# Kernel tuning notes

Hardware: AMD Instinct MI355X
Metric: run time of the kernel (lower is better)

Reference implementation:

```python
import jax, jax.numpy as jnp
import numpy as np

B, S, V, P = 16, 100, 50000, 45
WE, PE, H = 100, 50, 400
H2 = 2 * H  # bilstm output size


def _lstm(x, Wih, Whh, b):
    """Unidirectional LSTM over time. x: [B,S,D] -> h: [B,S,H]. PyTorch gate order i,f,g,o."""
    Hs = Whh.shape[1]
    def step(carry, xt):
        h, c = carry
        g = xt @ Wih.T + h @ Whh.T + b
        i, f, gg, o = jnp.split(g, 4, axis=-1)
        c = jax.nn.sigmoid(f) * c + jax.nn.sigmoid(i) * jnp.tanh(gg)
        h = jax.nn.sigmoid(o) * jnp.tanh(c)
        return (h, c), h
    Bn = x.shape[0]
    init = (jnp.zeros((Bn, Hs), x.dtype), jnp.zeros((Bn, Hs), x.dtype))
    _, hs = jax.lax.scan(step, init, jnp.swapaxes(x, 0, 1))
    return jnp.swapaxes(hs, 0, 1)


def _bilstm_layer(x, Wf_ih, Wf_hh, bf, Wb_ih, Wb_hh, bb):
    hf = _lstm(x, Wf_ih, Wf_hh, bf)
    hb = _lstm(x[:, ::-1, :], Wb_ih, Wb_hh, bb)[:, ::-1, :]
    return jnp.concatenate([hf, hb], axis=-1)


def setup_inputs() -> dict:
    key = jax.random.key(0)
    ks = jax.random.split(key, 24)
    def n(k, shape, s=0.1):
        return jax.random.normal(k, shape, jnp.float32) * s
    inp = {
        "input_tokens": jax.random.randint(ks[0], (B, S), 0, V),
        "input_pos": jax.random.randint(ks[1], (B, S), 0, P),
        "input_head": jax.random.randint(ks[2], (B, S), 0, S),
        "word_W": n(ks[3], (V, WE)),
        "pos_W": n(ks[4], (P, PE)),
        "l0f_Wih": n(ks[5], (4 * H, WE + PE)), "l0f_Whh": n(ks[6], (4 * H, H)), "l0f_b": n(ks[7], (4 * H,)),
        "l0b_Wih": n(ks[8], (4 * H, WE + PE)), "l0b_Whh": n(ks[9], (4 * H, H)), "l0b_b": n(ks[10], (4 * H,)),
        "l1f_Wih": n(ks[11], (4 * H, H2)), "l1f_Whh": n(ks[12], (4 * H, H)), "l1f_b": n(ks[13], (4 * H,)),
        "l1b_Wih": n(ks[14], (4 * H, H2)), "l1b_Whh": n(ks[15], (4 * H, H)), "l1b_b": n(ks[16], (4 * H,)),
        "ua_W": n(ks[17], (H2, H2)), "ua_b": n(ks[18], (H2,)),
        "wa_W": n(ks[19], (H2, H2)), "wa_b": n(ks[20], (H2,)),
        "va_W": n(ks[21], (H2,)),
    }
    return inp


def reference(input_tokens, input_pos, input_head, word_W, pos_W,
              l0f_Wih, l0f_Whh, l0f_b, l0b_Wih, l0b_Whh, l0b_b,
              l1f_Wih, l1f_Whh, l1f_b, l1b_Wih, l1b_Whh, l1b_b,
              ua_W, ua_b, wa_W, wa_b, va_W):
    # embeddings (dropout is identity at eval)
    x = jnp.concatenate([word_W[input_tokens], pos_W[input_pos]], axis=-1)  # [B,S,150]
    h1 = _bilstm_layer(x, l0f_Wih, l0f_Whh, l0f_b, l0b_Wih, l0b_Whh, l0b_b)   # [B,S,H2]
    out = _bilstm_layer(h1, l1f_Wih, l1f_Whh, l1f_b, l1b_Wih, l1b_Whh, l1b_b)  # [B,S,H2]

    # batched additive biaffine scoring for targets i = 1..S-1 over all source positions j
    ua = out @ ua_W.T + ua_b  # u_a(source)  [B,S,H2]
    wa = out @ wa_W.T + wa_b  # w_a(target)  [B,S,H2]
    # g[b,t,j] = v_a . tanh(ua[b,j] + wa[b,t+1])
    g = jnp.einsum('btjh,h->btj', jnp.tanh(ua[:, None, :, :] + wa[:, 1:, None, :]), va_W)  # [B,S-1,S]
    # mask: output[:, j, 0] == output[:, i, 0]  (masks self, matching torch's output.eq(target)[:,:,0])
    mask = out[:, 1:, 0][:, :, None] == out[:, :, 0][:, None, :]  # [B,S-1,S]
    g = jnp.where(mask, -10000.0, g)
    logp = jax.nn.log_softmax(g, axis=2)  # log_softmax over source positions (torch dim=1)

    # loss: sum over i of NLLLoss(mean over batch, ignore_index=-1)
    gold = input_head[:, 1:]  # [B,S-1]
    valid = (gold != -1)
    nll = -jnp.take_along_axis(logp, jnp.clip(gold, 0, S - 1)[:, :, None], axis=2)[..., 0]
    nll = nll * valid.astype(logp.dtype)
    denom = jnp.maximum(valid.sum(axis=0), 1).astype(logp.dtype)
    loss = jnp.sum(nll.sum(axis=0) / denom)

    parent_prob_table = jnp.exp(logp)  # [B,S-1,S]
    preds = jnp.argmax(parent_prob_table, axis=2)  # [B,S-1]
    return (loss, preds, parent_prob_table)
```

## Files before the change

kernel.cpp:

```cpp
#include <hip/hip_runtime.h>

#define BB 16
#define SS 100
#define HH 400
#define H2 800
#define G4 1600
#define DIN0 150
#define KP0 160

#define OFF_GF   240000ULL
#define OFF_GB   2800000ULL
#define OFF_H1   5360000ULL
#define OFF_OUT2 6640000ULL
#define OFF_NLL  8078400ULL
#define OFF_EXH  8081600ULL
#define EX_U16_PER_PLANE 1331200ULL

typedef _Float16 f16x8 __attribute__((ext_vector_type(8)));
typedef float    f32x4 __attribute__((ext_vector_type(4)));
typedef unsigned long long u64x2 __attribute__((ext_vector_type(2)));

static __device__ __forceinline__ unsigned chkp(unsigned long long q) {
    return ((unsigned)q == 0xFFFFFFFFu) | ((unsigned)(q >> 32) == 0xFFFFFFFFu);
}
static __device__ __forceinline__ unsigned long long sanq(unsigned long long q) {
    if ((unsigned)q == 0xFFFFFFFFu)         q &= 0xFFFFFFFF00000000ull;
    if ((unsigned)(q >> 32) == 0xFFFFFFFFu) q &= 0x00000000FFFFFFFFull;
    return q;
}

static __device__ __forceinline__ void cvt8(const float* v, f16x8& hi, f16x8& lo)
{
#pragma unroll
    for (int i = 0; i < 8; i++) {
        _Float16 h = (_Float16)v[i];
        hi[i] = h;
        lo[i] = (_Float16)((v[i] - (float)h) * 2048.f);
    }
}
static __device__ __forceinline__ void cvt_pair8(float4 a, float4 b,
                                                 f16x8& hi, f16x8& lo)
{
    float v[8] = {a.x, a.y, a.z, a.w, b.x, b.y, b.z, b.w};
    cvt8(v, hi, lo);
}

#define AROW 40

__global__ __launch_bounds__(256) void gemm_l0_embed_dual(
    const int* __restrict__ tok, const int* __restrict__ pos,
    const float* __restrict__ wW, const float* __restrict__ pW,
    const float* __restrict__ W0, const float* __restrict__ b0, float* __restrict__ C0,
    const float* __restrict__ W1, const float* __restrict__ b1, float* __restrict__ C1,
    unsigned int* __restrict__ poison, int poison_words)
{
    {
        int nthreads = gridDim.x * gridDim.y * 256;
        int gtid = (blockIdx.y * gridDim.x + blockIdx.x) * 256 + threadIdx.x;
        for (int i = gtid; i < poison_words; i += nthreads) poison[i] = 0xFFFFFFFFu;
    }

    int half = gridDim.x >> 1;
    int sel = blockIdx.x >= half;
    int bx = blockIdx.x - (sel ? half : 0);
    const float* W = sel ? W1 : W0;
    const float* bias = sel ? b1 : b0;
    float* C = sel ? C1 : C0;

    int tid = threadIdx.x;
    int wv = tid >> 6, l = tid & 63;
    int lm = l & 15, lk = l >> 4;
    int rs = bx * 64 + wv * 16;
    int n0 = blockIdx.y * 64;

    __shared__ __attribute__((aligned(16))) unsigned short AhiS[2][64 * AROW];
    __shared__ __attribute__((aligned(16))) unsigned short AloS[2][64 * AROW];

    int sr = tid >> 2, sc = (tid & 3) * 8;
    int t_ = tok[n0 + sr], p_ = pos[n0 + sr];

    const float* wrow = W + (size_t)(rs + lm) * DIN0;

    f32x4 accH[4], accX[4];
#pragma unroll
    for (int ct = 0; ct < 4; ct++) {
        accH[ct] = {0.f, 0.f, 0.f, 0.f};
        accX[ct] = {0.f, 0.f, 0.f, 0.f};
    }

    float a8[8];
#pragma unroll
    for (int e = 0; e < 8; e++) {
        int k = sc + e;
        a8[e] = (k < 100) ? wW[t_ * 100 + k]
              : (k < DIN0) ? pW[p_ * 50 + (k - 100)] : 0.f;
    }
    float w8[8];
#pragma unroll
    for (int e = 0; e < 8; e++) {
        int k = lk * 8 + e;
        w8[e] = (k < DIN0) ? wrow[k] : 0.f;
    }
    {
        f16x8 h, lo2; cvt8(a8, h, lo2);
        *(f16x8*)&AhiS[0][sr * AROW + sc] = h;
        *(f16x8*)&AloS[0][sr * AROW + sc] = lo2;
    }

    const int nkt = 5;
    for (int kt = 0; kt < nkt; kt++) {
        __syncthreads();
        bool more = (kt + 1 < nkt);
        float a8n[8], w8n[8];
        if (more) {
            int kb = (kt + 1) << 5;
#pragma unroll
            for (int e = 0; e < 8; e++) {
                int k = kb + sc + e;
                a8n[e] = (k < 100) ? wW[t_ * 100 + k]
                       : (k < DIN0) ? pW[p_ * 50 + (k - 100)] : 0.f;
            }
#pragma unroll
            for (int e = 0; e < 8; e++) {
                int k = kb + lk * 8 + e;
                w8n[e] = (k < DIN0) ? wrow[k] : 0.f;
            }
        }
        f16x8 wh, wl; cvt8(w8, wh, wl);
        int buf = kt & 1;
#pragma unroll
        for (int ct = 0; ct < 4; ct++) {
            f16x8 ah = *(const f16x8*)&AhiS[buf][(ct * 16 + lm) * AROW + lk * 8];
            f16x8 al = *(const f16x8*)&AloS[buf][(ct * 16 + lm) * AROW + lk * 8];
            accH[ct] = __builtin_amdgcn_mfma_f32_16x16x32_f16(wh, ah, accH[ct], 0, 0, 0);
            accX[ct] = __builtin_amdgcn_mfma_f32_16x16x32_f16(wh, al, accX[ct], 0, 0, 0);
            accX[ct] = __builtin_amdgcn_mfma_f32_16x16x32_f16(wl, ah, accX[ct], 0, 0, 0);
        }
        if (more) {
            f16x8 h, lo2; cvt8(a8n, h, lo2);
            *(f16x8*)&AhiS[buf ^ 1][sr * AROW + sc] = h;
            *(f16x8*)&AloS[buf ^ 1][sr * AROW + sc] = lo2;
#pragma unroll
            for (int e = 0; e < 8; e++) w8[e] = w8n[e];
        }
    }

    float4 bv = *(const float4*)&bias[rs + lk * 4];
#pragma unroll
    for (int ct = 0; ct < 4; ct++) {
        f32x4 v = accH[ct] + accX[ct] * (1.f / 2048.f);
        float4 o;
        o.x = v[0] + bv.x; o.y = v[1] + bv.y; o.z = v[2] + bv.z; o.w = v[3] + bv.w;
        *(float4*)&C[(size_t)(n0 + ct * 16 + lm) * G4 + rs + lk * 4] = o;
    }
}

__global__ __launch_bounds__(256) void gemm_nt_mfma_dual(
    const float* __restrict__ A,
    const float* __restrict__ W0, const float* __restrict__ b0, float* __restrict__ C0,
    const float* __restrict__ W1, const float* __restrict__ b1, float* __restrict__ C1,
    int K, int R,
    unsigned int* __restrict__ poison, int poison_words)
{
    if (poison) {
        int nthreads = gridDim.x * gridDim.y * 256;
        int gtid = (blockIdx.y * gridDim.x + blockIdx.x) * 256 + threadIdx.x;
        for (int i = gtid; i < poison_words; i += nthreads) poison[i] = 0xFFFFFFFFu;
    }

    int half = gridDim.x >> 1;
    int sel = blockIdx.x >= half;
    int bx = blockIdx.x - (sel ? half : 0);
    const float* W = sel ? W1 : W0;
    const float* bias = sel ? b1 : b0;
    float* C = sel ? C1 : C0;

    int tid = threadIdx.x;
    int wv = tid >> 6, l = tid & 63;
    int lm = l & 15, lk = l >> 4;
    int rs = bx * 64 + wv * 16;
    bool active = (rs < R);
    int n0 = blockIdx.y * 64;

    __shared__ __attribute__((aligned(16))) unsigned short AhiS[2][64 * AROW];
    __shared__ __attribute__((aligned(16))) unsigned short AloS[2][64 * AROW];

    int sr = tid >> 2, sc = (tid & 3) * 8;
    const float* arow_g = A + (size_t)(n0 + sr) * K + sc;
    const float* wrow = W + (size_t)((active ? rs : 0) + lm) * K + lk * 8;

    f32x4 accH[4], accX[4];
#pragma unroll
    for (int ct = 0; ct < 4; ct++) {
        accH[ct] = {0.f, 0.f, 0.f, 0.f};
        accX[ct] = {0.f, 0.f, 0.f, 0.f};
    }

    float a8[8];
    *(float4*)a8       = *(const float4*)arow_g;
    *(float4*)(a8 + 4) = *(const float4*)(arow_g + 4);
    float4 wA = {0,0,0,0}, wB = {0,0,0,0};
    if (active) { wA = *(const float4*)wrow; wB = *(const float4*)(wrow + 4); }
    {
        f16x8 h, lo2; cvt8(a8, h, lo2);
        *(f16x8*)&AhiS[0][sr * AROW + sc] = h;
        *(f16x8*)&AloS[0][sr * AROW + sc] = lo2;
    }

    int nkt = K >> 5;
    for (int kt = 0; kt < nkt; kt++) {
        __syncthreads();
        bool more = (kt + 1 < nkt);
        float a8n[8]; float4 wAn = {0,0,0,0}, wBn = {0,0,0,0};
        if (more) {
            int kb = (kt + 1) << 5;
            *(float4*)a8n       = *(const float4*)(arow_g + kb);
            *(float4*)(a8n + 4) = *(const float4*)(arow_g + kb + 4);
            if (active) {
                wAn = *(const float4*)(wrow + kb);
                wBn = *(const float4*)(wrow + kb + 4);
            }
        }
        if (active) {
            f16x8 wh, wl; cvt_pair8(wA, wB, wh, wl);
            int buf = kt & 1;
#pragma unroll
            for (int ct = 0; ct < 4; ct++) {
                f16x8 ah = *(const f16x8*)&AhiS[buf][(ct * 16 + lm) * AROW + lk * 8];
                f16x8 al = *(const f16x8*)&AloS[buf][(ct * 16 + lm) * AROW + lk * 8];
                accH[ct] = __builtin_amdgcn_mfma_f32_16x16x32_f16(wh, ah, accH[ct], 0, 0, 0);
                accX[ct] = __builtin_amdgcn_mfma_f32_16x16x32_f16(wh, al, accX[ct], 0, 0, 0);
                accX[ct] = __builtin_amdgcn_mfma_f32_16x16x32_f16(wl, ah, accX[ct], 0, 0, 0);
            }
        }
        if (more) {
            f16x8 h, lo2; cvt8(a8n, h, lo2);
            *(f16x8*)&AhiS[(kt & 1) ^ 1][sr * AROW + sc] = h;
            *(f16x8*)&AloS[(kt & 1) ^ 1][sr * AROW + sc] = lo2;
            wA = wAn; wB = wBn;
        }
    }

    if (!active) return;
    float4 bv = *(const float4*)&bias[rs + lk * 4];
#pragma unroll
    for (int ct = 0; ct < 4; ct++) {
        f32x4 v = accH[ct] + accX[ct] * (1.f / 2048.f);
        float4 o;
        o.x = v[0] + bv.x; o.y = v[1] + bv.y; o.z = v[2] + bv.z; o.w = v[3] + bv.w;
        *(float4*)&C[(size_t)(n0 + ct * 16 + lm) * R + rs + lk * 4] = o;
    }
}

__global__ __launch_bounds__(64, 1) void lstm_layer_kernel(
    const float* __restrict__ Gf, const float* __restrict__ Gb,
    const float* __restrict__ Wf, const float* __restrict__ Wb,
    float* __restrict__ hbuf,
    unsigned short* __restrict__ exhi,
    unsigned short* __restrict__ exlo)
{
    const int dir = blockIdx.x / 100;
    const int wg  = blockIdx.x % 100;
    const int j0  = wg * 4;
    const float* __restrict__ G = dir ? Gb : Gf;
    const float* __restrict__ W = dir ? Wb : Wf;

    const int l   = threadIdx.x;
    const int b   = l & 15;
    const int hi4 = l >> 4;

    __shared__ __attribute__((aligned(16))) unsigned short ahi[13 * 64 * 8];
    __shared__ __attribute__((aligned(16))) unsigned short alo[13 * 64 * 8];
    __shared__ float gl[16 * 17];

    {
        const int m = b;
        const int g = m >> 2, jj = m & 3;
        const float* wrow = W + (size_t)(g * HH + j0 + jj) * HH;
        for (int kt = 0; kt < 13; kt++) {
            for (int e = 0; e < 8; e++) {
                int k = kt * 32 + hi4 * 8 + e;
                float w = (k < HH) ? wrow[k] : 0.f;
                _Float16 wh = (_Float16)w;
                _Float16 wl = (_Float16)((w - (float)wh) * 2048.f);
                ahi[(kt * 64 + l) * 8 + e] = __builtin_bit_cast(unsigned short, wh);
                alo[(kt * 64 + l) * 8 + e] = __builtin_bit_cast(unsigned short, wl);
            }
        }
    }
    __syncthreads();

    float c_reg = 0.f;
    unsigned short* exh_d = exhi + (size_t)dir * 100 * 13 * 512;
    unsigned short* exl_d = exlo + (size_t)dir * 100 * 13 * 512;
    const int pad_lane = (hi4 >= 2);

    for (int s = 0; s < SS; s++) {
        const int time = dir ? (SS - 1 - s) : s;
        f32x4 gpre = *(const f32x4*)&G[(size_t)(b * SS + time) * G4 + hi4 * HH + j0];

        f32x4 acc;
        if (s > 0) {
            const unsigned long long* pbh =
                (const unsigned long long*)(exh_d + (size_t)(s - 1) * 13 * 512);
            const unsigned long long* pbl =
                (const unsigned long long*)(exl_d + (size_t)(s - 1) * 13 * 512);
            u64x2 vh2[13], vl2[13];
            vh2[12] = {0ull, 0ull};
            vl2[12] = {0ull, 0ull};
            unsigned bad = 1;
            for (int guard = 0; guard < (1 << 13); guard++) {
                bad = 0;
#pragma unroll
                for (int kt = 0; kt < 12; kt++) {
                    size_t q = (size_t)(kt * 64 + l) * 2;
                    vh2[kt][0] = __hip_atomic_load(pbh + q,     __ATOMIC_RELAXED, __HIP_MEMORY_SCOPE_AGENT);
                    vh2[kt][1] = __hip_atomic_load(pbh + q + 1, __ATOMIC_RELAXED, __HIP_MEMORY_SCOPE_AGENT);
                    vl2[kt][0] = __hip_atomic_load(pbl + q,     __ATOMIC_RELAXED, __HIP_MEMORY_SCOPE_AGENT);
                    vl2[kt][1] = __hip_atomic_load(pbl + q + 1, __ATOMIC_RELAXED, __HIP_MEMORY_SCOPE_AGENT);
                }
                if (!pad_lane) {
                    size_t q = (size_t)(12 * 64 + l) * 2;
                    vh2[12][0] = __hip_atomic_load(pbh + q,     __ATOMIC_RELAXED, __HIP_MEMORY_SCOPE_AGENT);
                    vh2[12][1] = __hip_atomic_load(pbh + q + 1, __ATOMIC_RELAXED, __HIP_MEMORY_SCOPE_AGENT);
                    vl2[12][0] = __hip_atomic_load(pbl + q,     __ATOMIC_RELAXED, __HIP_MEMORY_SCOPE_AGENT);
                    vl2[12][1] = __hip_atomic_load(pbl + q + 1, __ATOMIC_RELAXED, __HIP_MEMORY_SCOPE_AGENT);
                    bad |= chkp(vh2[12][0]) | chkp(vh2[12][1])
                         | chkp(vl2[12][0]) | chkp(vl2[12][1]);
                }
#pragma unroll
                for (int kt = 0; kt < 12; kt++) {
                    bad |= chkp(vh2[kt][0]) | chkp(vh2[kt][1])
                         | chkp(vl2[kt][0]) | chkp(vl2[kt][1]);
                }
                if (__ballot(bad != 0) == 0ull) break;
                __builtin_amdgcn_s_sleep(2);
            }
            if (bad) {
#pragma unroll
                for (int kt = 0; kt < 13; kt++) {
                    vh2[kt][0] = sanq(vh2[kt][0]); vh2[kt][1] = sanq(vh2[kt][1]);
                    vl2[kt][0] = sanq(vl2[kt][0]); vl2[kt][1] = sanq(vl2[kt][1]);
                }
            }
            asm volatile("" ::: "memory");

            f32x4 aHH = gpre;
            f32x4 aHL = {0.f, 0.f, 0.f, 0.f};
            f32x4 aLH = {0.f, 0.f, 0.f, 0.f};
#pragma unroll
            for (int kt = 0; kt < 13; kt++) {
                f16x8 bhv = __builtin_bit_cast(f16x8, vh2[kt]);
                f16x8 blv = __builtin_bit_cast(f16x8, vl2[kt]);
                f16x8 wh = *(const f16x8*)&ahi[(kt * 64 + l) * 8];
                f16x8 wl = *(const f16x8*)&alo[(kt * 64 + l) * 8];
                aHH = __builtin_amdgcn_mfma_f32_16x16x32_f16(wh, bhv, aHH, 0, 0, 0);
                aHL = __builtin_amdgcn_mfma_f32_16x16x32_f16(wh, blv, aHL, 0, 0, 0);
                aLH = __builtin_amdgcn_mfma_f32_16x16x32_f16(wl, bhv, aLH, 0, 0, 0);
            }
            acc = aHH + (aHL + aLH) * (1.f / 2048.f);
        } else {
            acc = gpre;
        }

#pragma unroll
        for (int q = 0; q < 4; q++) gl[(4 * hi4 + q) * 17 + b] = acc[q];
        __syncthreads();

        const int jj = hi4;
        float gi = gl[( 0 + jj) * 17 + b];
        float gf = gl[( 4 + jj) * 17 + b];
        float gg = gl[( 8 + jj) * 17 + b];
        float go = gl[(12 + jj) * 17 + b];
        __syncthreads();

        float si = 1.f / (1.f + expf(-gi));
        float sf = 1.f / (1.f + expf(-gf));
        float tg = tanhf(gg);
        float so = 1.f / (1.f + expf(-go));
        float c  = sf * c_reg + si * tg;
        c_reg = c;
        float h  = so * tanhf(c);

        if (s < SS - 1) {
            _Float16 hh = (_Float16)h;
            _Float16 hl = (_Float16)((h - (float)hh) * 2048.f);
            unsigned uh = __builtin_bit_cast(unsigned short, hh);
            unsigned ul = __builtin_bit_cast(unsigned short, hl);
            unsigned ph = uh | (((unsigned)__shfl_down((int)uh, 16)) << 16);
            unsigned pl = ul | (((unsigned)__shfl_down((int)ul, 16)) << 16);
            if ((jj & 1) == 0) {
                int k0 = j0 + jj;
                int kt = k0 >> 5, ko = k0 & 31;
                int lg = ko >> 3, e = ko & 7;
                size_t u16idx = ((size_t)(s * 13 + kt) * 64 + (lg * 16 + b)) * 8 + e;
                __hip_atomic_store((unsigned*)(exh_d + u16idx), ph,
                                   __ATOMIC_RELAXED, __HIP_MEMORY_SCOPE_AGENT);
                __hip_atomic_store((unsigned*)(exl_d + u16idx), pl,
                                   __ATOMIC_RELAXED, __HIP_MEMORY_SCOPE_AGENT);
            }
        }

        hbuf[(size_t)(b * SS + time) * H2 + dir * HH + j0 + jj] = h;
    }
}

#define ITILE 7
#define NTILE 15
__global__ __launch_bounds__(256) void attn_scores_softmax_kernel(
    const float* __restrict__ ua, const float* __restrict__ wa,
    const float* __restrict__ va, const float* __restrict__ out2,
    const int* __restrict__ head, float* __restrict__ outb,
    float* __restrict__ nll)
{
    int b  = blockIdx.x / NTILE;
    int i0 = (blockIdx.x % NTILE) * ITILE;
    int tid = threadIdx.x;
    __shared__ float ua_t[100][101];
    __shared__ float wa_t[ITILE][102];
    __shared__ float sacc[ITILE][101];
    __shared__ float va_t[100];
    __shared__ float h0[100];

    for (int p = tid; p < ITILE * 101; p += 256) ((float*)sacc)[p] = 0.f;
    if (tid < 100) h0[tid] = out2[(size_t)(b * SS + tid) * H2];

    for (int ht = 0; ht < 8; ht++) {
        int hh0 = ht * 100;
        __syncthreads();
        for (int p = tid; p < 100 * 100; p += 256) {
            int j = p / 100, hh = p % 100;
            ua_t[j][hh] = ua[(size_t)(b * SS + j) * H2 + hh0 + hh];
        }
        for (int p = tid; p < ITILE * 100; p += 256) {
            int il = p / 100, hh = p % 100;
            wa_t[il][hh] = (i0 + il + 1 < SS)
                ? wa[(size_t)(b * SS + i0 + il + 1) * H2 + hh0 + hh] : 0.f;
        }
        if (tid < 100) va_t[tid] = va[hh0 + tid];
        __syncthreads();
        for (int p = tid; p < ITILE * 100; p += 256) {
            int il = p / 100, j = p % 100;
            float acc = 0.f;
#pragma unroll 4
            for (int hh = 0; hh < 100; hh++) {
                float x = ua_t[j][hh] + wa_t[il][hh];
                float z = __expf(2.f * x);
                float th = 1.f - 2.f * __builtin_amdgcn_rcpf(z + 1.f);
                acc = fmaf(th, va_t[hh], acc);
            }
            sacc[il][j] += acc;
        }
    }
    __syncthreads();

    int wv = tid >> 6, ln = tid & 63;
    for (int il = wv; il < ITILE; il += 4) {
        int i = i0 + il;
        if (i > 98) continue;
        int bi = b * 99 + i;
        float h_t = h0[i + 1];
        int j1 = ln, j2 = ln + 64;
        float s1 = sacc[il][j1];
        if (h0[j1] == h_t) s1 = -10000.0f;
        float s2 = -1e30f;
        if (j2 < 100) {
            s2 = sacc[il][j2];
            if (h0[j2] == h_t) s2 = -10000.0f;
        }
        float v = s1; int vi = j1;
        if (s2 > v) { v = s2; vi = j2; }
        for (int k = 32; k >= 1; k >>= 1) {
            float vo = __shfl_xor(v, k);
            int   io = __shfl_xor(vi, k);
            if (vo > v || (vo == v && io < vi)) { v = vo; vi = io; }
        }
        float m = v; int amax = vi;
        float e1 = __expf(s1 - m);
        float e2 = (j2 < 100) ? __expf(s2 - m) : 0.f;
        float sum = e1 + e2;
        for (int k = 32; k >= 1; k >>= 1) sum += __shfl_xor(sum, k);
        float inv = 1.f / sum;
        outb[1 + 1584 + (size_t)bi * 100 + j1] = e1 * inv;
        if (j2 < 100) outb[1 + 1584 + (size_t)bi * 100 + j2] = e2 * inv;
        if (ln == 0) {
            outb[1 + bi] = (float)amax;
            int gold = head[b * SS + i + 1];
            bool valid = (gold != -1);
            int gc = gold < 0 ? 0 : (gold > 99 ? 99 : gold);
            float sgc = sacc[il][gc];
            if (h0[gc] == h_t) sgc = -10000.0f;
            nll[bi] = valid ? -(sgc - m - logf(sum)) : 0.f;
        }
    }
}

__global__ __launch_bounds__(128) void loss_kernel(
    const float* __restrict__ nll, const int* __restrict__ head,
    float* __restrict__ outb)
{
    __shared__ float red[128];
    int tid = threadIdx.x;
    float contrib = 0.f;
    if (tid < 99) {
        int i = tid;
        float tot = 0.f; int cv = 0;
        for (int b = 0; b < BB; b++) {
            tot += nll[b * 99 + i];
            cv += (head[b * SS + i + 1] != -1) ? 1 : 0;
        }
        int denom = cv > 0 ? cv : 1;
        contrib = tot / (float)denom;
    }
    red[tid] = contrib;
    __syncthreads();
    for (int off = 64; off >= 1; off >>= 1) {
        if (tid < off) red[tid] += red[tid + off];
        __syncthreads();
    }
    if (tid == 0) outb[0] = red[0];
}

extern "C" void kernel_launch(void* const* d_in, const int* in_sizes, int n_in,
                              void* d_out, int out_size, void* d_ws, size_t ws_size,
                              hipStream_t stream) {
    const int*   tok     = (const int*)d_in[0];
    const int*   pos     = (const int*)d_in[1];
    const int*   head    = (const int*)d_in[2];
    const float* word_W  = (const float*)d_in[3];
    const float* pos_W   = (const float*)d_in[4];
    const float* l0f_Wih = (const float*)d_in[5];
    const float* l0f_Whh = (const float*)d_in[6];
    const float* l0f_b   = (const float*)d_in[7];
    const float* l0b_Wih = (const float*)d_in[8];
    const float* l0b_Whh = (const float*)d_in[9];
    const float* l0b_b   = (const float*)d_in[10];
    const float* l1f_Wih = (const float*)d_in[11];
    const float* l1f_Whh = (const float*)d_in[12];
    const float* l1f_b   = (const float*)d_in[13];
    const float* l1b_Wih = (const float*)d_in[14];
    const float* l1b_Whh = (const float*)d_in[15];
    const float* l1b_b   = (const float*)d_in[16];
    const float* ua_W    = (const float*)d_in[17];
    const float* ua_b    = (const float*)d_in[18];
    const float* wa_W    = (const float*)d_in[19];
    const float* wa_b    = (const float*)d_in[20];
    const float* va_W    = (const float*)d_in[21];

    float* ws   = (float*)d_ws;
    float* gf   = ws + OFF_GF;
    float* gb   = ws + OFF_GB;
    float* h1   = ws + OFF_H1;
    float* out2 = ws + OFF_OUT2;
    float* nllb = ws + OFF_NLL;
    unsigned short* exhi = (unsigned short*)(ws + OFF_EXH);
    unsigned short* exlo = exhi + EX_U16_PER_PLANE;
    float* outf = (float*)d_out;

    gemm_l0_embed_dual<<<dim3(50, 25), 256, 0, stream>>>(
        tok, pos, word_W, pos_W,
        l0f_Wih, l0f_b, gf, l0b_Wih, l0b_b, gb,
        (unsigned int*)exhi, (int)EX_U16_PER_PLANE);
    lstm_layer_kernel<<<dim3(200), 64, 0, stream>>>(
        gf, gb, l0f_Whh, l0b_Whh, h1, exhi, exlo);
    gemm_nt_mfma_dual<<<dim3(50, 25), 256, 0, stream>>>(
        h1, l1f_Wih, l1f_b, gf, l1b_Wih, l1b_b, gb, H2, G4,
        (unsigned int*)exhi, (int)EX_U16_PER_PLANE);
    lstm_layer_kernel<<<dim3(200), 64, 0, stream>>>(
        gf, gb, l1f_Whh, l1b_Whh, out2, exhi, exlo);
    gemm_nt_mfma_dual<<<dim3(26, 25), 256, 0, stream>>>(
        out2, ua_W, ua_b, gf, wa_W, wa_b, gb, H2, H2, nullptr, 0);
    attn_scores_softmax_kernel<<<dim3(BB * NTILE), 256, 0, stream>>>(
        gf, gb, va_W, out2, head, outf, nllb);
    loss_kernel<<<dim3(1), 128, 0, stream>>>(nllb, head, outf);
}
```

Before: 1.224 ms.

## Assign eight hidden units per LSTM workgroup, halving the persistent grid

The persistent recurrent LSTM kernel now gives each workgroup 8 hidden units instead of 4, so it launches 100 workgroups instead of 200. Each workgroup runs two MFMA tile sets per step over the same loaded h vector. This halves the number of workgroups that poll and read the exchanged hidden state through global memory each step, cutting cross-workgroup traffic and sync contention. The cost is twice the per-step compute and LDS weight storage per workgroup, so the serial critical path per step gets longer.

```diff
diff --git a/kernel.cpp b/kernel.cpp
--- a/kernel.cpp
+++ b/kernel.cpp
@@ -7,6 +7,7 @@
 #define G4 1600
 #define DIN0 150
 #define KP0 160
+#define LWG 50
 
 #define OFF_GF   240000ULL
 #define OFF_GB   2800000ULL
@@ -259,9 +260,9 @@
     unsigned short* __restrict__ exhi,
     unsigned short* __restrict__ exlo)
 {
-    const int dir = blockIdx.x / 100;
-    const int wg  = blockIdx.x % 100;
-    const int j0  = wg * 4;
+    const int dir = blockIdx.x / LWG;
+    const int wg  = blockIdx.x % LWG;
+    const int j0  = wg * 8;
     const float* __restrict__ G = dir ? Gb : Gf;
     const float* __restrict__ W = dir ? Wb : Wf;
 
@@ -269,37 +270,38 @@
     const int b   = l & 15;
     const int hi4 = l >> 4;
 
-    __shared__ __attribute__((aligned(16))) unsigned short ahi[13 * 64 * 8];
-    __shared__ __attribute__((aligned(16))) unsigned short alo[13 * 64 * 8];
-    __shared__ float gl[16 * 17];
-
-    {
-        const int m = b;
-        const int g = m >> 2, jj = m & 3;
-        const float* wrow = W + (size_t)(g * HH + j0 + jj) * HH;
+    __shared__ __attribute__((aligned(16))) unsigned short ahi[2][13 * 64 * 8];
+    __shared__ __attribute__((aligned(16))) unsigned short alo[2][13 * 64 * 8];
+    __shared__ float gl[32 * 17];
+
+    for (int t = 0; t < 2; t++) {
+        const int g = b >> 2, jj = b & 3;
+        const float* wrow = W + (size_t)(g * HH + j0 + t * 4 + jj) * HH;
         for (int kt = 0; kt < 13; kt++) {
             for (int e = 0; e < 8; e++) {
                 int k = kt * 32 + hi4 * 8 + e;
                 float w = (k < HH) ? wrow[k] : 0.f;
                 _Float16 wh = (_Float16)w;
                 _Float16 wl = (_Float16)((w - (float)wh) * 2048.f);
-                ahi[(kt * 64 + l) * 8 + e] = __builtin_bit_cast(unsigned short, wh);
-                alo[(kt * 64 + l) * 8 + e] = __builtin_bit_cast(unsigned short, wl);
+                ahi[t][(kt * 64 + l) * 8 + e] = __builtin_bit_cast(unsigned short, wh);
+                alo[t][(kt * 64 + l) * 8 + e] = __builtin_bit_cast(unsigned short, wl);
             }
         }
     }
     __syncthreads();
 
-    float c_reg = 0.f;
+    float c0 = 0.f, c1 = 0.f;
     unsigned short* exh_d = exhi + (size_t)dir * 100 * 13 * 512;
     unsigned short* exl_d = exlo + (size_t)dir * 100 * 13 * 512;
     const int pad_lane = (hi4 >= 2);
 
     for (int s = 0; s < SS; s++) {
         const int time = dir ? (SS - 1 - s) : s;
-        f32x4 gpre = *(const f32x4*)&G[(size_t)(b * SS + time) * G4 + hi4 * HH + j0];
-
-        f32x4 acc;
+        const float* gbase = &G[(size_t)(b * SS + time) * G4 + hi4 * HH + j0];
+        f32x4 gpre0 = *(const f32x4*)gbase;
+        f32x4 gpre1 = *(const f32x4*)(gbase + 4);
+
+        f32x4 acc0, acc1;
         if (s > 0) {
             const unsigned long long* pbh =
                 (const unsigned long long*)(exh_d + (size_t)(s - 1) * 13 * 512);
@@ -345,63 +347,99 @@
             }
             asm volatile("" ::: "memory");
 
-            f32x4 aHH = gpre;
-            f32x4 aHL = {0.f, 0.f, 0.f, 0.f};
-            f32x4 aLH = {0.f, 0.f, 0.f, 0.f};
+            f32x4 aHH0 = gpre0, aHL0 = {0,0,0,0}, aLH0 = {0,0,0,0};
+            f32x4 aHH1 = gpre1, aHL1 = {0,0,0,0}, aLH1 = {0,0,0,0};
 #pragma unroll
             for (int kt = 0; kt < 13; kt++) {
                 f16x8 bhv = __builtin_bit_cast(f16x8, vh2[kt]);
                 f16x8 blv = __builtin_bit_cast(f16x8, vl2[kt]);
-                f16x8 wh = *(const f16x8*)&ahi[(kt * 64 + l) * 8];
-                f16x8 wl = *(const f16x8*)&alo[(kt * 64 + l) * 8];
-                aHH = __builtin_amdgcn_mfma_f32_16x16x32_f16(wh, bhv, aHH, 0, 0, 0);
-                aHL = __builtin_amdgcn_mfma_f32_16x16x32_f16(wh, blv, aHL, 0, 0, 0);
-                aLH = __builtin_amdgcn_mfma_f32_16x16x32_f16(wl, bhv, aLH, 0, 0, 0);
-            }
-            acc = aHH + (aHL + aLH) * (1.f / 2048.f);
+                int base = (kt * 64 + l) * 8;
+                f16x8 wh0 = *(const f16x8*)&ahi[0][base];
+                f16x8 wl0 = *(const f16x8*)&alo[0][base];
+                f16x8 wh1 = *(const f16x8*)&ahi[1][base];
+                f16x8 wl1 = *(const f16x8*)&alo[1][base];
+                aHH0 = __builtin_amdgcn_mfma_f32_16x16x32_f16(wh0, bhv, aHH0, 0, 0, 0);
+                aHL0 = __builtin_amdgcn_mfma_f32_16x16x32_f16(wh0, blv, aHL0, 0, 0, 0);
+                aLH0 = __builtin_amdgcn_mfma_f32_16x16x32_f16(wl0, bhv, aLH0, 0, 0, 0);
+                aHH1 = __builtin_amdgcn_mfma_f32_16x16x32_f16(wh1, bhv, aHH1, 0, 0, 0);
+                aHL1 = __builtin_amdgcn_mfma_f32_16x16x32_f16(wh1, blv, aHL1, 0, 0, 0);
+                aLH1 = __builtin_amdgcn_mfma_f32_16x16x32_f16(wl1, bhv, aLH1, 0, 0, 0);
+            }
+            acc0 = aHH0 + (aHL0 + aLH0) * (1.f / 2048.f);
+            acc1 = aHH1 + (aHL1 + aLH1) * (1.f / 2048.f);
         } else {
-            acc = gpre;
-        }
-
-#pragma unroll
-        for (int q = 0; q < 4; q++) gl[(4 * hi4 + q) * 17 + b] = acc[q];
+            acc0 = gpre0;
+            acc1 = gpre1;
+        }
+
+#pragma unroll
+        for (int q = 0; q < 4; q++) {
+            gl[(hi4 * 8 + q)     * 17 + b] = acc0[q];
+            gl[(hi4 * 8 + 4 + q) * 17 + b] = acc1[q];
+        }
         __syncthreads();
 
-        const int jj = hi4;
-        float gi = gl[( 0 + jj) * 17 + b];
-        float gf = gl[( 4 + jj) * 17 + b];
-        float gg = gl[( 8 + jj) * 17 + b];
-        float go = gl[(12 + jj) * 17 + b];
+        float h0v, h1v;
+        {
+            const int u0 = hi4;
+            float gi = gl[( 0 + u0) * 17 + b];
+            float gf = gl[( 8 + u0) * 17 + b];
+            float gg = gl[(16 + u0) * 17 + b];
+            float go = gl[(24 + u0) * 17 + b];
+            float si = 1.f / (1.f + expf(-gi));
+            float sf = 1.f / (1.f + expf(-gf));
+            float tg = tanhf(gg);
+            float so = 1.f / (1.f + expf(-go));
+            c0 = sf * c0 + si * tg;
+            h0v = so * tanhf(c0);
+            const int u1 = hi4 + 4;
+            float gi1 = gl[( 0 + u1) * 17 + b];
+            float gf1 = gl[( 8 + u1) * 17 + b];
+            float gg1 = gl[(16 + u1) * 17 + b];
+            float go1 = gl[(24 + u1) * 17 + b];
+            float si1 = 1.f / (1.f + expf(-gi1));
+            float sf1 = 1.f / (1.f + expf(-gf1));
+            float tg1 = tanhf(gg1);
+            float so1 = 1.f / (1.f + expf(-go1));
+            c1 = sf1 * c1 + si1 * tg1;
+            h1v = so1 * tanhf(c1);
+        }
         __syncthreads();
 
-        float si = 1.f / (1.f + expf(-gi));
-        float sf = 1.f / (1.f + expf(-gf));
-        float tg = tanhf(gg);
-        float so = 1.f / (1.f + expf(-go));
-        float c  = sf * c_reg + si * tg;
-        c_reg = c;
-        float h  = so * tanhf(c);
-
         if (s < SS - 1) {
-            _Float16 hh = (_Float16)h;
-            _Float16 hl = (_Float16)((h - (float)hh) * 2048.f);
-            unsigned uh = __builtin_bit_cast(unsigned short, hh);
-            unsigned ul = __builtin_bit_cast(unsigned short, hl);
-            unsigned ph = uh | (((unsigned)__shfl_down((int)uh, 16)) << 16);
-            unsigned pl = ul | (((unsigned)__shfl_down((int)ul, 16)) << 16);
-            if ((jj & 1) == 0) {
-                int k0 = j0 + jj;
-                int kt = k0 >> 5, ko = k0 & 31;
-                int lg = ko >> 3, e = ko & 7;
-                size_t u16idx = ((size_t)(s * 13 + kt) * 64 + (lg * 16 + b)) * 8 + e;
-                __hip_atomic_store((unsigned*)(exh_d + u16idx), ph,
+            _Float16 hh0 = (_Float16)h0v;
+            _Float16 hl0 = (_Float16)((h0v - (float)hh0) * 2048.f);
+            _Float16 hh1 = (_Float16)h1v;
+            _Float16 hl1 = (_Float16)((h1v - (float)hh1) * 2048.f);
+            unsigned uh0 = __builtin_bit_cast(unsigned short, hh0);
+            unsigned ul0 = __builtin_bit_cast(unsigned short, hl0);
+            unsigned uh1 = __builtin_bit_cast(unsigned short, hh1);
+            unsigned ul1 = __builtin_bit_cast(unsigned short, hl1);
+            unsigned ph0 = uh0 | (((unsigned)__shfl_down((int)uh0, 16)) << 16);
+            unsigned pl0 = ul0 | (((unsigned)__shfl_down((int)ul0, 16)) << 16);
+            unsigned ph1 = uh1 | (((unsigned)__shfl_down((int)uh1, 16)) << 16);
+            unsigned pl1 = ul1 | (((unsigned)__shfl_down((int)ul1, 16)) << 16);
+            if ((hi4 & 1) == 0) {
+                int k0a = j0 + hi4;
+                int kta = k0a >> 5, koa = k0a & 31;
+                size_t ia = ((size_t)(s * 13 + kta) * 64 + ((koa >> 3) * 16 + b)) * 8 + (koa & 7);
+                __hip_atomic_store((unsigned*)(exh_d + ia), ph0,
                                    __ATOMIC_RELAXED, __HIP_MEMORY_SCOPE_AGENT);
-                __hip_atomic_store((unsigned*)(exl_d + u16idx), pl,
+                __hip_atomic_store((unsigned*)(exl_d + ia), pl0,
                                    __ATOMIC_RELAXED, __HIP_MEMORY_SCOPE_AGENT);
-            }
-        }
-
-        hbuf[(size_t)(b * SS + time) * H2 + dir * HH + j0 + jj] = h;
+                int k0b = j0 + 4 + hi4;
+                int ktb = k0b >> 5, kob = k0b & 31;
+                size_t ib = ((size_t)(s * 13 + ktb) * 64 + ((kob >> 3) * 16 + b)) * 8 + (kob & 7);
+                __hip_atomic_store((unsigned*)(exh_d + ib), ph1,
+                                   __ATOMIC_RELAXED, __HIP_MEMORY_SCOPE_AGENT);
+                __hip_atomic_store((unsigned*)(exl_d + ib), pl1,
+                                   __ATOMIC_RELAXED, __HIP_MEMORY_SCOPE_AGENT);
+            }
+        }
+
+        size_t hb = (size_t)(b * SS + time) * H2 + dir * HH + j0 + hi4;
+        hbuf[hb]     = h0v;
+        hbuf[hb + 4] = h1v;
     }
 }
 
@@ -561,12 +599,12 @@
         tok, pos, word_W, pos_W,
         l0f_Wih, l0f_b, gf, l0b_Wih, l0b_b, gb,
         (unsigned int*)exhi, (int)EX_U16_PER_PLANE);
-    lstm_layer_kernel<<<dim3(200), 64, 0, stream>>>(
+    lstm_layer_kernel<<<dim3(2 * LWG), 64, 0, stream>>>(
         gf, gb, l0f_Whh, l0b_Whh, h1, exhi, exlo);
     gemm_nt_mfma_dual<<<dim3(50, 25), 256, 0, stream>>>(
         h1, l1f_Wih, l1f_b, gf, l1b_Wih, l1b_b, gb, H2, G4,
         (unsigned int*)exhi, (int)EX_U16_PER_PLANE);
-    lstm_layer_kernel<<<dim3(200), 64, 0, stream>>>(
+    lstm_layer_kernel<<<dim3(2 * LWG), 64, 0, stream>>>(
         gf, gb, l1f_Whh, l1b_Whh, out2, exhi, exlo);
     gemm_nt_mfma_dual<<<dim3(26, 25), 256, 0, stream>>>(
         out2, ua_W, ua_b, gf, wa_W, wa_b, gb, H2, H2, nullptr, 0);
```

Measured after the change: 1.406 ms. 1.15x slower.
